# Kernel tuning notes

Hardware: AMD Instinct MI355X
Metric: run time of the kernel (lower is better)

## Reference

```python
import jax, jax.numpy as jnp
import numpy as np

EPS = 1e-5  # InstanceNorm2d default eps


def setup_inputs() -> dict:
    key = jax.random.key(0)
    k1, k2, k3, k4, k5 = jax.random.split(key, 5)
    B2, N, C = 16, 1024, 128
    H = 8
    CH = C * H
    emb = jax.random.normal(k1, (B2, N, C), dtype=jnp.float32)
    # torch nn.Linear weight layout: [out_features, in_features]
    s = 1.0 / np.sqrt(C)
    Wq = jax.random.uniform(k2, (CH, C), dtype=jnp.float32, minval=-s, maxval=s)
    Wk = jax.random.uniform(k3, (CH, C), dtype=jnp.float32, minval=-s, maxval=s)
    Wv = jax.random.uniform(k4, (CH, C), dtype=jnp.float32, minval=-s, maxval=s)
    so = 1.0 / np.sqrt(CH)
    Wo = jax.random.uniform(k5, (C, CH), dtype=jnp.float32, minval=-so, maxval=so)
    return {"emb": emb, "Wq": Wq, "Wk": Wk, "Wv": Wv, "Wo": Wo}


def reference(emb, Wq, Wk, Wv, Wo):
    B2, N, C = emb.shape
    B = B2 // 2
    emb_s, emb_t = emb[:B], emb[B:]

    q = emb_s @ Wq.T              # [B, N, CH]
    k = emb_t @ Wk.T              # [B, N, CH]
    v = emb_t @ Wv.T              # [B, N, CH]

    CH = q.shape[-1]
    # rearrange 'b n c -> n (b c)': keys/values shared across all source batches
    k_flat = k.transpose(1, 0, 2).reshape(N, B * CH)   # [N, B*CH]
    v_flat = v.transpose(1, 0, 2).reshape(N, B * CH)   # [N, B*CH]

    # q^T @ k : attention over channel dims -> scores [B, CH, B*CH]
    scores = jnp.einsum('bnc,nd->bcd', q, k_flat)

    # InstanceNorm2d on [B, 1, CH, B*CH]: normalize over the whole score map
    # per batch element (single channel), biased variance, no affine.
    mean = jnp.mean(scores, axis=(1, 2), keepdims=True)
    var = jnp.var(scores, axis=(1, 2), keepdims=True)
    scores = (scores - mean) * jax.lax.rsqrt(var + EPS)

    attn = jax.nn.softmax(scores, axis=-1)             # softmax over B*CH
    # (dropout is identity in eval mode / rate 0)

    ctx = jnp.einsum('bcd,nd->bnc', attn, v_flat)      # [B, N, CH]
    out = ctx @ Wo.T                                   # [B, N, C]
    return out
```

## Files before the change

### kernel.cpp

```cpp
#include <hip/hip_runtime.h>
#include <stdint.h>

typedef unsigned short u16;
typedef __attribute__((ext_vector_type(8))) short short8;
typedef __attribute__((ext_vector_type(8))) __bf16 bf16x8;
typedef __attribute__((ext_vector_type(4))) float f32x4;
typedef __attribute__((ext_vector_type(4))) u16 u16x4;

#define CDINV (1.0f / 8388608.0f)

__device__ __forceinline__ u16 f2b(float f) {
  union { float f; unsigned u; } v; v.f = f;
  unsigned r = (v.u + 0x7FFFu + ((v.u >> 16) & 1u)) >> 16;
  return (u16)r;
}
__device__ __forceinline__ float b2f(u16 h) {
  union { unsigned u; float f; } v; v.u = ((unsigned)h) << 16;
  return v.f;
}

__device__ __forceinline__ void gll16(const void* g, void* l) {
  __builtin_amdgcn_global_load_lds((const __attribute__((address_space(1))) void*)g,
                                   (__attribute__((address_space(3))) void*)l, 16, 0, 0);
}

__device__ __forceinline__ void gemm_core(const u16* __restrict__ Ab, int lda,
                                          const u16* __restrict__ Bb, int ldb,
                                          int ksteps,
                                          u16 (&ldsA)[4096], u16 (&ldsB)[4096],
                                          f32x4 acc[4][4]) {
  const int t = threadIdx.x;
  const int w = t >> 6, l = t & 63;
  const int wr = (w >> 1) << 6, wc = (w & 1) << 6;
  const int srow = (w << 4) + (l >> 2);
  const int skk = (l & 3) << 3;
  const int fr = l & 15;
  const int fk = (l >> 4) << 3;
  for (int ks = 0; ks < ksteps; ++ks) {
    const int k0 = ks << 5;
    __syncthreads();
#pragma unroll
    for (int i = 0; i < 2; ++i) {
      gll16(Ab + (size_t)(i * 64 + srow) * (size_t)lda + (size_t)k0 + skk,
            ldsA + i * 2048 + w * 512);
      gll16(Bb + (size_t)(i * 64 + srow) * (size_t)ldb + (size_t)k0 + skk,
            ldsB + i * 2048 + w * 512);
    }
    __syncthreads();
    bf16x8 af[4], bfv[4];
#pragma unroll
    for (int m = 0; m < 4; ++m)
      af[m] = __builtin_bit_cast(bf16x8,
              *(const short8*)(ldsA + (wr + m * 16 + fr) * 32 + fk));
#pragma unroll
    for (int n = 0; n < 4; ++n)
      bfv[n] = __builtin_bit_cast(bf16x8,
              *(const short8*)(ldsB + (wc + n * 16 + fr) * 32 + fk));
#pragma unroll
    for (int m = 0; m < 4; ++m)
#pragma unroll
      for (int n = 0; n < 4; ++n)
        acc[m][n] = __builtin_amdgcn_mfma_f32_16x16x32_bf16(af[m], bfv[n],
                                                            acc[m][n], 0, 0, 0);
  }
}

__global__ __launch_bounds__(256) void k_convert(
    const float* __restrict__ emb, const float* __restrict__ wq,
    const float* __restrict__ wk, const float* __restrict__ wv,
    const float* __restrict__ wo, u16* __restrict__ embB, u16* __restrict__ wqB,
    u16* __restrict__ wkB, u16* __restrict__ wvB, u16* __restrict__ woB,
    float* __restrict__ S) {
  int i = blockIdx.x * 256 + threadIdx.x;
  if (i < 16) S[i] = 0.0f;
  if (i < 2097152) { embB[i] = f2b(emb[i]); return; }
  int j = i - 2097152;
  if (j < 131072) { wqB[j] = f2b(wq[j]); return; }
  j -= 131072;
  if (j < 131072) { wkB[j] = f2b(wk[j]); return; }
  j -= 131072;
  if (j < 131072) { wvB[j] = f2b(wv[j]); return; }
  j -= 131072;
  if (j < 131072) { woB[j] = f2b(wo[j]); return; }
}

__global__ __launch_bounds__(256) void k_proj(
    const u16* __restrict__ embB, const u16* __restrict__ wqB,
    const u16* __restrict__ wkB, const u16* __restrict__ wvB,
    u16* __restrict__ qT, u16* __restrict__ kT, u16* __restrict__ vb) {
  __shared__ u16 ldsA[4096], ldsB[4096];
  const int x = blockIdx.x, b = blockIdx.y, mat = blockIdx.z;
  const int n0 = (x & 7) << 7, ch0 = (x >> 3) << 7;
  const int rowbase = ((mat == 0 ? b : b + 8) << 10) + n0;
  const u16* W = (mat == 0) ? wqB : ((mat == 1) ? wkB : wvB);
  f32x4 acc[4][4];
#pragma unroll
  for (int m = 0; m < 4; ++m)
#pragma unroll
    for (int n = 0; n < 4; ++n) acc[m][n] = (f32x4){0.f, 0.f, 0.f, 0.f};
  gemm_core(embB + (size_t)rowbase * 128, 128, W + (size_t)ch0 * 128, 128, 4,
            ldsA, ldsB, acc);
  const int t = threadIdx.x, w = t >> 6, l = t & 63;
  const int wr = (w >> 1) << 6, wc = (w & 1) << 6;
  if (mat < 2) {
    u16* dst = (mat == 0 ? qT : kT) + (size_t)b * 1048576u;
#pragma unroll
    for (int m = 0; m < 4; ++m)
#pragma unroll
      for (int n = 0; n < 4; ++n) {
        int rl = wr + m * 16 + ((l >> 4) << 2);
        int cl = wc + n * 16 + (l & 15);
        u16x4 pk;
#pragma unroll
        for (int j = 0; j < 4; ++j) pk[j] = f2b(acc[m][n][j]);
        *(u16x4*)(dst + (size_t)(ch0 + cl) * 1024u + (size_t)(n0 + rl)) = pk;
      }
  } else {
    u16* dst = vb + (size_t)b * 1048576u;
#pragma unroll
    for (int m = 0; m < 4; ++m)
#pragma unroll
      for (int n = 0; n < 4; ++n) {
        int rl = wr + m * 16 + ((l >> 4) << 2);
        int cl = wc + n * 16 + (l & 15);
#pragma unroll
        for (int j = 0; j < 4; ++j)
          dst[(size_t)(n0 + rl + j) * 1024u + (size_t)(ch0 + cl)] = f2b(acc[m][n][j]);
      }
  }
}

__global__ __launch_bounds__(512, 2) void k_qk2(const u16* __restrict__ qT,
                                                const u16* __restrict__ kT,
                                                u16* __restrict__ sc,
                                                float* __restrict__ S) {
  __shared__ u16 lds[32768];
  char* ldsb = (char*)lds;
  const int bid = blockIdx.x;
  const int mt = (bid & 7) * 4 + (bid >> 8);
  const int nt = (bid >> 3) & 31;
  const int t = threadIdx.x, w = t >> 6, l = t & 63;
  const int wm = w >> 2, wn = w & 3;
  const int fr = l & 15, fq = l >> 4;
  const int sr0 = w * 16 + (l >> 2);
  const int kk = (l & 3) << 3;
  const int lbase = w * 1024;
  const u16* A0 = qT + (size_t)(mt * 256 + sr0) * 1024u + kk;
  const u16* B0 = kT + (size_t)(nt * 256 + sr0) * 1024u + kk;
  const int ard = (wm * 128 + fr) * 64 + fq * 16;
  const int brd = 16384 + (wn * 64 + fr) * 64 + fq * 16;

  f32x4 acc[8][4];
#pragma unroll
  for (int m = 0; m < 8; ++m)
#pragma unroll
    for (int n = 0; n < 4; ++n) acc[m][n] = (f32x4){0.f, 0.f, 0.f, 0.f};

#define QK_STAGE(s_, p_)                                                    \
  {                                                                         \
    const int k0_ = (s_) << 5;                                              \
    char* la_ = ldsb + (p_) * 32768 + lbase;                                \
    gll16(A0 + k0_, la_);                                                   \
    gll16(A0 + k0_ + 131072, la_ + 8192);                                   \
    char* lb_ = ldsb + (p_) * 32768 + 16384 + lbase;                        \
    gll16(B0 + k0_, lb_);                                                   \
    gll16(B0 + k0_ + 131072, lb_ + 8192);                                   \
  }

  QK_STAGE(0, 0);
  __syncthreads();
  for (int s = 0; s < 32; ++s) {
    const int p = s & 1;
    if (s < 31) QK_STAGE(s + 1, p ^ 1);
    char* base = ldsb + p * 32768;
    bf16x8 af[8], bfv[4];
#pragma unroll
    for (int m = 0; m < 8; ++m)
      af[m] = __builtin_bit_cast(bf16x8, *(const short8*)(base + ard + m * 1024));
#pragma unroll
    for (int n = 0; n < 4; ++n)
      bfv[n] = __builtin_bit_cast(bf16x8, *(const short8*)(base + brd + n * 1024));
#pragma unroll
    for (int m = 0; m < 8; ++m)
#pragma unroll
      for (int n = 0; n < 4; ++n)
        acc[m][n] = __builtin_amdgcn_mfma_f32_16x16x32_bf16(af[m], bfv[n],
                                                            acc[m][n], 0, 0, 0);
    __syncthreads();
  }
#undef QK_STAGE

  const int mrow0 = mt * 256 + wm * 128 + fq * 4;
  const int ncol0 = nt * 256 + wn * 64 + fr;
  const int b = mt >> 2;
  float ls = 0.f, lq = 0.f;
#pragma unroll
  for (int m = 0; m < 8; ++m)
#pragma unroll
    for (int n = 0; n < 4; ++n) {
      const int row = mrow0 + m * 16;
      const int col = ncol0 + n * 16;
#pragma unroll
      for (int j = 0; j < 4; ++j) {
        float sv = acc[m][n][j];
        ls += sv; lq += sv * sv;
        sc[(size_t)(row + j) * 8192u + (size_t)col] = f2b(sv);
      }
    }
#pragma unroll
  for (int off = 32; off; off >>= 1) {
    ls += __shfl_down(ls, off);
    lq += __shfl_down(lq, off);
  }
  if (l == 0) { atomicAdd(&S[b], ls); atomicAdd(&S[8 + b], lq); }
}

__global__ void k_stats(const float* __restrict__ S, float* __restrict__ r) {
  int t = threadIdx.x;
  if (t < 8) {
    float mean = S[t] * CDINV;
    float var = S[8 + t] * CDINV - mean * mean;
    r[t] = rsqrtf(var + 1e-5f);
  }
}

__global__ __launch_bounds__(256) void k_softmax(u16* __restrict__ sc,
                                                 const float* __restrict__ rb) {
  const int wg = blockIdx.x;
  const int b = wg >> 10, c = wg & 1023;
  u16* rowp = sc + (size_t)b * 8388608u + (size_t)c * 8192u;
  const float rl = rb[b] * 1.44269504089f;
  const int t = threadIdx.x, w = t >> 6, l = t & 63;
  __shared__ float red[4];
  __shared__ float bcast;
  float v[4][8];
  float m = -1e30f;
#pragma unroll
  for (int i = 0; i < 4; ++i) {
    short8 x = *(const short8*)(rowp + i * 2048 + t * 8);
#pragma unroll
    for (int j = 0; j < 8; ++j) {
      v[i][j] = b2f((u16)x[j]);
      m = fmaxf(m, v[i][j]);
    }
  }
#pragma unroll
  for (int off = 32; off; off >>= 1) m = fmaxf(m, __shfl_xor(m, off));
  if (l == 0) red[w] = m;
  __syncthreads();
  if (t == 0) bcast = fmaxf(fmaxf(red[0], red[1]), fmaxf(red[2], red[3]));
  __syncthreads();
  m = bcast;
  float s = 0.f;
#pragma unroll
  for (int i = 0; i < 4; ++i)
#pragma unroll
    for (int j = 0; j < 8; ++j) {
      v[i][j] = exp2f((v[i][j] - m) * rl);
      s += v[i][j];
    }
#pragma unroll
  for (int off = 32; off; off >>= 1) s += __shfl_xor(s, off);
  __syncthreads();
  if (l == 0) red[w] = s;
  __syncthreads();
  if (t == 0) bcast = 1.0f / (red[0] + red[1] + red[2] + red[3]);
  __syncthreads();
  const float inv = bcast;
#pragma unroll
  for (int i = 0; i < 4; ++i) {
    short8 x;
#pragma unroll
    for (int j = 0; j < 8; ++j) x[j] = (short)f2b(v[i][j] * inv);
    *(short8*)(rowp + i * 2048 + t * 8) = x;
  }
}

__global__ __launch_bounds__(512, 2) void k_pv2(const u16* __restrict__ vb,
                                                const u16* __restrict__ sc,
                                                u16* __restrict__ ctx) {
  __shared__ u16 lds[24576];
  char* ldsb = (char*)lds;
  const int bid = blockIdx.x;
  const int nt = ((bid & 7) << 2) | (bid >> 6);
  const int mt = (bid >> 3) & 7;
  const int t = threadIdx.x, w = t >> 6, l = t & 63;
  const int wm = w >> 2, wn = w & 3;
  const int fr = l & 15, fq = l >> 4;
  const int sr0 = w * 16 + (l >> 2);
  const int kk = (l & 3) << 3;
  const int lbase = w * 1024;
  const u16* Abase = vb + (size_t)(mt * 128 + sr0) * 1024u + kk;
  const u16* B0 = sc + (size_t)(nt * 256 + sr0) * 8192u + kk;
  const int ard = (wm * 64 + fr) * 64 + fq * 16;
  const int brd = 8192 + (wn * 64 + fr) * 64 + fq * 16;

  f32x4 acc[4][4];
#pragma unroll
  for (int m = 0; m < 4; ++m)
#pragma unroll
    for (int n = 0; n < 4; ++n) acc[m][n] = (f32x4){0.f, 0.f, 0.f, 0.f};

#define PV_STAGE(s_, p_)                                                     \
  {                                                                          \
    const int k0_ = (s_) << 5;                                               \
    gll16(Abase + (size_t)(k0_ >> 10) * 1048576u + (k0_ & 1023),             \
          ldsb + (p_) * 24576 + lbase);                                      \
    char* lb_ = ldsb + (p_) * 24576 + 8192 + lbase;                          \
    gll16(B0 + k0_, lb_);                                                    \
    gll16(B0 + k0_ + 1048576, lb_ + 8192);                                   \
  }

  PV_STAGE(0, 0);
  __syncthreads();
  for (int s = 0; s < 256; ++s) {
    const int p = s & 1;
    if (s < 255) PV_STAGE(s + 1, p ^ 1);
    char* base = ldsb + p * 24576;
    bf16x8 af[4], bfv[4];
#pragma unroll
    for (int m = 0; m < 4; ++m)
      af[m] = __builtin_bit_cast(bf16x8, *(const short8*)(base + ard + m * 1024));
#pragma unroll
    for (int n = 0; n < 4; ++n)
      bfv[n] = __builtin_bit_cast(bf16x8, *(const short8*)(base + brd + n * 1024));
#pragma unroll
    for (int m = 0; m < 4; ++m)
#pragma unroll
      for (int n = 0; n < 4; ++n)
        acc[m][n] = __builtin_amdgcn_mfma_f32_16x16x32_bf16(af[m], bfv[n],
                                                            acc[m][n], 0, 0, 0);
    __syncthreads();
  }
#undef PV_STAGE

  const int b = nt >> 2;
  u16* dstb = ctx + (size_t)b * 1048576u;
  const int nrow0 = mt * 128 + wm * 64 + fq * 4;
  const int c0 = ((nt & 3) << 8) + wn * 64 + fr;
#pragma unroll
  for (int m = 0; m < 4; ++m)
#pragma unroll
    for (int n = 0; n < 4; ++n) {
      const int nrow = nrow0 + m * 16;
      const int c = c0 + n * 16;
#pragma unroll
      for (int j = 0; j < 4; ++j)
        dstb[(size_t)(nrow + j) * 1024u + (size_t)c] = f2b(acc[m][n][j]);
    }
}

__global__ __launch_bounds__(256) void k_out(const u16* __restrict__ ctx,
                                             const u16* __restrict__ woB,
                                             float* __restrict__ out) {
  __shared__ u16 ldsA[4096], ldsB[4096];
  const int x = blockIdx.x;
  f32x4 acc[4][4];
#pragma unroll
  for (int m = 0; m < 4; ++m)
#pragma unroll
    for (int n = 0; n < 4; ++n) acc[m][n] = (f32x4){0.f, 0.f, 0.f, 0.f};
  gemm_core(ctx + (size_t)x * 128u * 1024u, 1024, woB, 1024, 32, ldsA, ldsB, acc);
  const int t = threadIdx.x, w = t >> 6, l = t & 63;
  const int wr = (w >> 1) << 6, wc = (w & 1) << 6;
#pragma unroll
  for (int m = 0; m < 4; ++m)
#pragma unroll
    for (int n = 0; n < 4; ++n) {
      int rl = wr + m * 16 + ((l >> 4) << 2);
      int cl = wc + n * 16 + (l & 15);
      if (cl < 128) {
#pragma unroll
        for (int j = 0; j < 4; ++j)
          out[(size_t)(x * 128 + rl + j) * 128u + (size_t)cl] = acc[m][n][j];
      }
    }
}

extern "C" void kernel_launch(void* const* d_in, const int* in_sizes, int n_in,
                              void* d_out, int out_size, void* d_ws, size_t ws_size,
                              hipStream_t stream) {
  const float* emb = (const float*)d_in[0];
  const float* wq = (const float*)d_in[1];
  const float* wk = (const float*)d_in[2];
  const float* wv = (const float*)d_in[3];
  const float* wo = (const float*)d_in[4];
  float* out = (float*)d_out;

  char* w = (char*)d_ws;
  u16* sc = (u16*)w;
  u16* qT = (u16*)(w + 134217728);
  u16* kT = qT + 8388608;
  u16* vb = kT + 8388608;
  u16* embB = vb + 8388608;
  u16* wqB = embB + 2097152;
  u16* wkB = wqB + 131072;
  u16* wvB = wkB + 131072;
  u16* woB = wvB + 131072;
  float* S = (float*)(woB + 131072);
  float* r = S + 16;
  u16* ctx = qT;

  k_convert<<<10240, 256, 0, stream>>>(emb, wq, wk, wv, wo, embB, wqB, wkB, wvB,
                                       woB, S);
  k_proj<<<dim3(64, 8, 3), 256, 0, stream>>>(embB, wqB, wkB, wvB, qT, kT, vb);
  k_qk2<<<1024, 512, 0, stream>>>(qT, kT, sc, S);
  k_stats<<<1, 64, 0, stream>>>(S, r);
  k_softmax<<<8192, 256, 0, stream>>>(sc, r);
  k_pv2<<<256, 512, 0, stream>>>(vb, sc, ctx);
  k_out<<<64, 256, 0, stream>>>(ctx, woB, out);
}
```

Measured before the change: 626.2 us.

## Swizzle LDS tiles and use vmcnt-based double buffering in QK and PV GEMMs

Both GEMM kernels now XOR-swizzle the 16-byte chunk position of each row, on the global-to-LDS load side and on the fragment-read side, to reduce LDS bank conflicts. The main loops are restructured with explicit s_barrier, sched_barrier and partial s_waitcnt vmcnt, so the next stage's async loads stay in flight while the current buffer is consumed, and the last iteration is peeled. The goal is to overlap memory latency with MFMA work and cut the stalls from the full __syncthreads waits. The risk is in the hand-placed waitcnt counts and barriers, where an error would cause data races.

New measurement: 598.4 us. 4.4% less time.

```diff
diff --git a/kernel.cpp b/kernel.cpp
--- a/kernel.cpp
+++ b/kernel.cpp
@@ -130,6 +130,24 @@
   }
 }
 
+
+__device__ __forceinline__ void qk_compute(char* base, int ard, int brd,
+                                           f32x4 (&acc)[8][4]) {
+  bf16x8 af[8], bfv[4];
+#pragma unroll
+  for (int m = 0; m < 8; ++m)
+    af[m] = __builtin_bit_cast(bf16x8, *(const short8*)(base + ard + m * 1024));
+#pragma unroll
+  for (int n = 0; n < 4; ++n)
+    bfv[n] = __builtin_bit_cast(bf16x8, *(const short8*)(base + brd + n * 1024));
+#pragma unroll
+  for (int m = 0; m < 8; ++m)
+#pragma unroll
+    for (int n = 0; n < 4; ++n)
+      acc[m][n] = __builtin_amdgcn_mfma_f32_16x16x32_bf16(af[m], bfv[n],
+                                                          acc[m][n], 0, 0, 0);
+}
+
 __global__ __launch_bounds__(512, 2) void k_qk2(const u16* __restrict__ qT,
                                                 const u16* __restrict__ kT,
                                                 u16* __restrict__ sc,
@@ -143,12 +161,13 @@
   const int wm = w >> 2, wn = w & 3;
   const int fr = l & 15, fq = l >> 4;
   const int sr0 = w * 16 + (l >> 2);
-  const int kk = (l & 3) << 3;
+  const int kk = (((l & 3) ^ ((l >> 4) & 3)) << 3);
   const int lbase = w * 1024;
   const u16* A0 = qT + (size_t)(mt * 256 + sr0) * 1024u + kk;
   const u16* B0 = kT + (size_t)(nt * 256 + sr0) * 1024u + kk;
-  const int ard = (wm * 128 + fr) * 64 + fq * 16;
-  const int brd = 16384 + (wn * 64 + fr) * 64 + fq * 16;
+  const int swz = ((fq ^ (fr >> 2)) << 4);
+  const int ard = (wm * 128 + fr) * 64 + swz;
+  const int brd = 16384 + (wn * 64 + fr) * 64 + swz;
 
   f32x4 acc[8][4];
 #pragma unroll
@@ -168,26 +187,26 @@
   }
 
   QK_STAGE(0, 0);
-  __syncthreads();
-  for (int s = 0; s < 32; ++s) {
+  for (int s = 0; s < 31; ++s) {
     const int p = s & 1;
-    if (s < 31) QK_STAGE(s + 1, p ^ 1);
-    char* base = ldsb + p * 32768;
-    bf16x8 af[8], bfv[4];
-#pragma unroll
-    for (int m = 0; m < 8; ++m)
-      af[m] = __builtin_bit_cast(bf16x8, *(const short8*)(base + ard + m * 1024));
-#pragma unroll
-    for (int n = 0; n < 4; ++n)
-      bfv[n] = __builtin_bit_cast(bf16x8, *(const short8*)(base + brd + n * 1024));
-#pragma unroll
-    for (int m = 0; m < 8; ++m)
-#pragma unroll
-      for (int n = 0; n < 4; ++n)
-        acc[m][n] = __builtin_amdgcn_mfma_f32_16x16x32_bf16(af[m], bfv[n],
-                                                            acc[m][n], 0, 0, 0);
-    __syncthreads();
-  }
+    __builtin_amdgcn_s_barrier();
+    __builtin_amdgcn_sched_barrier(0);
+    QK_STAGE(s + 1, p ^ 1);
+    asm volatile("s_waitcnt vmcnt(4)" ::: "memory");
+    __builtin_amdgcn_sched_barrier(0);
+    __builtin_amdgcn_s_barrier();
+    __builtin_amdgcn_sched_barrier(0);
+    asm volatile("" ::: "memory");
+    qk_compute(ldsb + p * 32768, ard, brd, acc);
+  }
+  __builtin_amdgcn_s_barrier();
+  __builtin_amdgcn_sched_barrier(0);
+  asm volatile("s_waitcnt vmcnt(0)" ::: "memory");
+  __builtin_amdgcn_sched_barrier(0);
+  __builtin_amdgcn_s_barrier();
+  __builtin_amdgcn_sched_barrier(0);
+  asm volatile("" ::: "memory");
+  qk_compute(ldsb + 32768, ard, brd, acc);
 #undef QK_STAGE
 
   const int mrow0 = mt * 256 + wm * 128 + fq * 4;
@@ -274,6 +293,23 @@
     for (int j = 0; j < 8; ++j) x[j] = (short)f2b(v[i][j] * inv);
     *(short8*)(rowp + i * 2048 + t * 8) = x;
   }
+}
+
+__device__ __forceinline__ void pv_compute(char* base, int ard, int brd,
+                                           f32x4 (&acc)[4][4]) {
+  bf16x8 af[4], bfv[4];
+#pragma unroll
+  for (int m = 0; m < 4; ++m)
+    af[m] = __builtin_bit_cast(bf16x8, *(const short8*)(base + ard + m * 1024));
+#pragma unroll
+  for (int n = 0; n < 4; ++n)
+    bfv[n] = __builtin_bit_cast(bf16x8, *(const short8*)(base + brd + n * 1024));
+#pragma unroll
+  for (int m = 0; m < 4; ++m)
+#pragma unroll
+    for (int n = 0; n < 4; ++n)
+      acc[m][n] = __builtin_amdgcn_mfma_f32_16x16x32_bf16(af[m], bfv[n],
+                                                          acc[m][n], 0, 0, 0);
 }
 
 __global__ __launch_bounds__(512, 2) void k_pv2(const u16* __restrict__ vb,
@@ -288,12 +324,13 @@
   const int wm = w >> 2, wn = w & 3;
   const int fr = l & 15, fq = l >> 4;
   const int sr0 = w * 16 + (l >> 2);
-  const int kk = (l & 3) << 3;
+  const int kk = (((l & 3) ^ ((l >> 4) & 3)) << 3);
   const int lbase = w * 1024;
   const u16* Abase = vb + (size_t)(mt * 128 + sr0) * 1024u + kk;
   const u16* B0 = sc + (size_t)(nt * 256 + sr0) * 8192u + kk;
-  const int ard = (wm * 64 + fr) * 64 + fq * 16;
-  const int brd = 8192 + (wn * 64 + fr) * 64 + fq * 16;
+  const int swz = ((fq ^ (fr >> 2)) << 4);
+  const int ard = (wm * 64 + fr) * 64 + swz;
+  const int brd = 8192 + (wn * 64 + fr) * 64 + swz;
 
   f32x4 acc[4][4];
 #pragma unroll
@@ -312,26 +349,26 @@
   }
 
   PV_STAGE(0, 0);
-  __syncthreads();
-  for (int s = 0; s < 256; ++s) {
+  for (int s = 0; s < 255; ++s) {
     const int p = s & 1;
-    if (s < 255) PV_STAGE(s + 1, p ^ 1);
-    char* base = ldsb + p * 24576;
-    bf16x8 af[4], bfv[4];
-#pragma unroll
-    for (int m = 0; m < 4; ++m)
-      af[m] = __builtin_bit_cast(bf16x8, *(const short8*)(base + ard + m * 1024));
-#pragma unroll
-    for (int n = 0; n < 4; ++n)
-      bfv[n] = __builtin_bit_cast(bf16x8, *(const short8*)(base + brd + n * 1024));
-#pragma unroll
-    for (int m = 0; m < 4; ++m)
-#pragma unroll
-      for (int n = 0; n < 4; ++n)
-        acc[m][n] = __builtin_amdgcn_mfma_f32_16x16x32_bf16(af[m], bfv[n],
-                                                            acc[m][n], 0, 0, 0);
-    __syncthreads();
-  }
+    __builtin_amdgcn_s_barrier();
+    __builtin_amdgcn_sched_barrier(0);
+    PV_STAGE(s + 1, p ^ 1);
+    asm volatile("s_waitcnt vmcnt(3)" ::: "memory");
+    __builtin_amdgcn_sched_barrier(0);
+    __builtin_amdgcn_s_barrier();
+    __builtin_amdgcn_sched_barrier(0);
+    asm volatile("" ::: "memory");
+    pv_compute(ldsb + p * 24576, ard, brd, acc);
+  }
+  __builtin_amdgcn_s_barrier();
+  __builtin_amdgcn_sched_barrier(0);
+  asm volatile("s_waitcnt vmcnt(0)" ::: "memory");
+  __builtin_amdgcn_sched_barrier(0);
+  __builtin_amdgcn_s_barrier();
+  __builtin_amdgcn_sched_barrier(0);
+  asm volatile("" ::: "memory");
+  pv_compute(ldsb + 24576, ard, brd, acc);
 #undef PV_STAGE
 
   const int b = nt >> 2;
```

## Swizzle PV LDS tiles, hand-schedule PV pipeline, fold stats into softmax

Applied to the files above, without the earlier changes.

Applies an XOR swizzle to the LDS layout of the PV GEMM tiles, both when loading from global and when reading fragments, to reduce bank conflicts. The PV main loop is restructured with explicit s_barrier, vmcnt waits and sched_barriers so the next stage's global-to-LDS loads overlap the current compute, with the final stage peeled. The separate stats kernel is removed; each softmax block computes mean and rstd from the accumulated sums itself. This saves one launch but adds a little redundant scalar work per block, and the manual waitcnt ordering is fragile.

Result: faster. 580.8 us (-7.2%).

```diff
diff --git a/kernel.cpp b/kernel.cpp
--- a/kernel.cpp
+++ b/kernel.cpp
@@ -215,21 +215,14 @@
   if (l == 0) { atomicAdd(&S[b], ls); atomicAdd(&S[8 + b], lq); }
 }
 
-__global__ void k_stats(const float* __restrict__ S, float* __restrict__ r) {
-  int t = threadIdx.x;
-  if (t < 8) {
-    float mean = S[t] * CDINV;
-    float var = S[8 + t] * CDINV - mean * mean;
-    r[t] = rsqrtf(var + 1e-5f);
-  }
-}
-
 __global__ __launch_bounds__(256) void k_softmax(u16* __restrict__ sc,
-                                                 const float* __restrict__ rb) {
+                                                 const float* __restrict__ S) {
   const int wg = blockIdx.x;
   const int b = wg >> 10, c = wg & 1023;
   u16* rowp = sc + (size_t)b * 8388608u + (size_t)c * 8192u;
-  const float rl = rb[b] * 1.44269504089f;
+  const float mean = S[b] * CDINV;
+  const float var = S[8 + b] * CDINV - mean * mean;
+  const float rl = rsqrtf(var + 1e-5f) * 1.44269504089f;
   const int t = threadIdx.x, w = t >> 6, l = t & 63;
   __shared__ float red[4];
   __shared__ float bcast;
@@ -274,6 +267,23 @@
     for (int j = 0; j < 8; ++j) x[j] = (short)f2b(v[i][j] * inv);
     *(short8*)(rowp + i * 2048 + t * 8) = x;
   }
+}
+
+__device__ __forceinline__ void pv_compute(char* base, int ard, int brd,
+                                           f32x4 (&acc)[4][4]) {
+  bf16x8 af[4], bfv[4];
+#pragma unroll
+  for (int m = 0; m < 4; ++m)
+    af[m] = __builtin_bit_cast(bf16x8, *(const short8*)(base + ard + m * 1024));
+#pragma unroll
+  for (int n = 0; n < 4; ++n)
+    bfv[n] = __builtin_bit_cast(bf16x8, *(const short8*)(base + brd + n * 1024));
+#pragma unroll
+  for (int m = 0; m < 4; ++m)
+#pragma unroll
+    for (int n = 0; n < 4; ++n)
+      acc[m][n] = __builtin_amdgcn_mfma_f32_16x16x32_bf16(af[m], bfv[n],
+                                                          acc[m][n], 0, 0, 0);
 }
 
 __global__ __launch_bounds__(512, 2) void k_pv2(const u16* __restrict__ vb,
@@ -288,12 +298,13 @@
   const int wm = w >> 2, wn = w & 3;
   const int fr = l & 15, fq = l >> 4;
   const int sr0 = w * 16 + (l >> 2);
-  const int kk = (l & 3) << 3;
+  const int kk = (((l & 3) ^ ((l >> 4) & 3)) << 3);
   const int lbase = w * 1024;
   const u16* Abase = vb + (size_t)(mt * 128 + sr0) * 1024u + kk;
   const u16* B0 = sc + (size_t)(nt * 256 + sr0) * 8192u + kk;
-  const int ard = (wm * 64 + fr) * 64 + fq * 16;
-  const int brd = 8192 + (wn * 64 + fr) * 64 + fq * 16;
+  const int swz = ((fq ^ (fr >> 2)) << 4);
+  const int ard = (wm * 64 + fr) * 64 + swz;
+  const int brd = 8192 + (wn * 64 + fr) * 64 + swz;
 
   f32x4 acc[4][4];
 #pragma unroll
@@ -312,26 +323,26 @@
   }
 
   PV_STAGE(0, 0);
-  __syncthreads();
-  for (int s = 0; s < 256; ++s) {
+  for (int s = 0; s < 255; ++s) {
     const int p = s & 1;
-    if (s < 255) PV_STAGE(s + 1, p ^ 1);
-    char* base = ldsb + p * 24576;
-    bf16x8 af[4], bfv[4];
-#pragma unroll
-    for (int m = 0; m < 4; ++m)
-      af[m] = __builtin_bit_cast(bf16x8, *(const short8*)(base + ard + m * 1024));
-#pragma unroll
-    for (int n = 0; n < 4; ++n)
-      bfv[n] = __builtin_bit_cast(bf16x8, *(const short8*)(base + brd + n * 1024));
-#pragma unroll
-    for (int m = 0; m < 4; ++m)
-#pragma unroll
-      for (int n = 0; n < 4; ++n)
-        acc[m][n] = __builtin_amdgcn_mfma_f32_16x16x32_bf16(af[m], bfv[n],
-                                                            acc[m][n], 0, 0, 0);
-    __syncthreads();
-  }
+    __builtin_amdgcn_s_barrier();
+    __builtin_amdgcn_sched_barrier(0);
+    PV_STAGE(s + 1, p ^ 1);
+    asm volatile("s_waitcnt vmcnt(3)" ::: "memory");
+    __builtin_amdgcn_sched_barrier(0);
+    __builtin_amdgcn_s_barrier();
+    __builtin_amdgcn_sched_barrier(0);
+    asm volatile("" ::: "memory");
+    pv_compute(ldsb + p * 24576, ard, brd, acc);
+  }
+  __builtin_amdgcn_s_barrier();
+  __builtin_amdgcn_sched_barrier(0);
+  asm volatile("s_waitcnt vmcnt(0)" ::: "memory");
+  __builtin_amdgcn_sched_barrier(0);
+  __builtin_amdgcn_s_barrier();
+  __builtin_amdgcn_sched_barrier(0);
+  asm volatile("" ::: "memory");
+  pv_compute(ldsb + 24576, ard, brd, acc);
 #undef PV_STAGE
 
   const int b = nt >> 2;
@@ -398,15 +409,13 @@
   u16* wvB = wkB + 131072;
   u16* woB = wvB + 131072;
   float* S = (float*)(woB + 131072);
-  float* r = S + 16;
   u16* ctx = qT;
 
   k_convert<<<10240, 256, 0, stream>>>(emb, wq, wk, wv, wo, embB, wqB, wkB, wvB,
                                        woB, S);
   k_proj<<<dim3(64, 8, 3), 256, 0, stream>>>(embB, wqB, wkB, wvB, qT, kT, vb);
   k_qk2<<<1024, 512, 0, stream>>>(qT, kT, sc, S);
-  k_stats<<<1, 64, 0, stream>>>(S, r);
-  k_softmax<<<8192, 256, 0, stream>>>(sc, r);
+  k_softmax<<<8192, 256, 0, stream>>>(sc, S);
   k_pv2<<<256, 512, 0, stream>>>(vb, sc, ctx);
   k_out<<<64, 256, 0, stream>>>(ctx, woB, out);
 }
```
